# Kernel optimization log

Hardware: AMD Instinct MI355X
Metric: run time of the kernel (lower is better)

The kernel has to match this reference:

```python
import jax, jax.numpy as jnp
import numpy as np

N, F, E = 65536, 64, 16   # batch, fields, embedding_size
H1, H2 = 8, 4             # hidden_dims
BN_EPS = 1e-5


def setup_inputs() -> dict:
    key = jax.random.key(0)
    ks = jax.random.split(key, 12)
    rn = lambda k, shape, sc=1.0: jax.random.normal(k, shape, dtype=jnp.float32) * sc
    return {
        "Xa": rn(ks[0], (N, F)),
        "Xc": rn(ks[1], (N, F)),
        # per-field Linear(1,1) weights/biases (two first-order embedding lists)
        "w1": rn(ks[2], (F,)), "b1": rn(ks[3], (F,)),
        "w2": rn(ks[4], (F,)), "b2": rn(ks[5], (F,)),
        # per-field Linear(1,E) weights/biases (two second-order embedding lists)
        "W1": rn(ks[6], (F, E)), "B1": rn(ks[7], (F, E)),
        "W2": rn(ks[8], (F, E)), "B2": rn(ks[9], (F, E)),
        # deep MLP: linear_1 (F*E -> 8) + BN, linear_2 (8 -> 4). No final layer (init bug).
        "lin1_w": rn(ks[10], (H1, F * E), 0.01), "lin1_b": jnp.zeros((H1,), jnp.float32),
        "bn1_gamma": jnp.ones((H1,), jnp.float32), "bn1_beta": jnp.zeros((H1,), jnp.float32),
        "lin2_w": rn(ks[11], (H2, H1), 0.01), "lin2_b": jnp.full((H2,), 0.21, jnp.float32),
    }


def reference(Xa, Xc, w1, b1, w2, b2, W1, B1, W2, B2,
              lin1_w, lin1_b, bn1_gamma, bn1_beta, lin2_w, lin2_b):
    n = Xa.shape[0]
    # ---- FM first order (faithful to the torch broadcast: arr_2[i] is (N,N)
    # with entry [r,c] = Xa[r,i]*(w2[i]*Xc[c,i]+b2[i]); only mean over the
    # concat dim is consumed, so compute the column-mean analytically). ----
    first1 = (w1 * Xa + b1) * Xc                         # (N,F)
    xc_mean = jnp.mean(Xc, axis=0)                       # (F,)
    first2_cmean = Xa * (w2 * xc_mean + b2)              # (N,F) = mean over c of arr_2
    fm_first_mean = jnp.mean(first1 + first2_cmean, axis=1, keepdims=True)  # (N,1)

    # ---- FM second order: per-field (N,E) embeddings, fully batched. ----
    Xa3 = Xa[:, :, None]                                 # (N,F,1)
    Xc3 = Xc[:, :, None]
    emb = (Xa3 * W1 + B1) * Xc3 + Xa3 * (W2 * Xc3 + B2)  # (N,F,E)
    s = emb.sum(axis=1)                                  # (N,E)
    fm_second = 0.5 * (s * s - (emb * emb).sum(axis=1))  # (N,E)
    fm_second_mean = jnp.mean(fm_second, axis=1, keepdims=True)  # (N,1)

    # ---- deep part: cat of per-field (N,E) -> (N, F*E), field-major. ----
    deep = emb.reshape(n, F * E)
    h = deep @ lin1_w.T + lin1_b                         # (N,8)
    mu = h.mean(axis=0)
    var = h.var(axis=0)                                  # biased, as BN training mode
    h = (h - mu) / jnp.sqrt(var + BN_EPS) * bn1_gamma + bn1_beta
    h = jnp.tanh(h)                                      # dropout = identity (eval)
    h = h @ lin2_w.T + lin2_b                            # (N,4) — no final projection (init bug)
    deep_mean = h.mean(axis=1, keepdims=True)            # (N,1)

    return fm_first_mean + fm_second_mean + deep_mean    # (N,1)
```

## Files before the change

kernel.cpp:

```cpp
#include <hip/hip_runtime.h>
#include <math.h>

#define NROWS 65536
#define BN_EPS 1e-5f
#define NBLK   512

#define OFF_PARTIAL 0
#define OFF_H       65536
#define OFF_REC     589824
#define OFF_BLKT    595200
#define OFF_T       636160

__global__ __launch_bounds__(64) void precompute_kernel(
    const float* __restrict__ W1, const float* __restrict__ B1,
    const float* __restrict__ W2, const float* __restrict__ B2,
    const float* __restrict__ lin1_w, const float* __restrict__ w1,
    const float* __restrict__ b1, const float* __restrict__ b2,
    float* __restrict__ rec)
{
    int f = blockIdx.x, t = threadIdx.x;
    __shared__ float u[16], x[16], y[16];
    if (t < 16) {
        float uu = W1[f * 16 + t] + W2[f * 16 + t];
        float xx = B1[f * 16 + t];
        float yy = B2[f * 16 + t];
        u[t] = uu; x[t] = xx; y[t] = yy;
        rec[f * 84 + t]      = uu;
        rec[f * 84 + 16 + t] = xx;
        rec[f * 84 + 32 + t] = yy;
    }
    __syncthreads();
    if (t < 24) {
        int j = t & 7, which = t >> 3;
        const float* src = (which == 0) ? u : (which == 1) ? x : y;
        const float* lw = lin1_w + j * 1024 + f * 16;
        float acc = 0.f;
#pragma unroll
        for (int e = 0; e < 16; e++) acc = fmaf(src[e], lw[e], acc);
        rec[f * 84 + 48 + which * 8 + j] = acc;
    } else if (t < 30) {
        int q = t - 24;
        const float* s1 = (q == 0 || q == 3 || q == 4) ? u : (q == 1 || q == 5) ? x : y;
        const float* s2 = (q == 0) ? u : (q == 1 || q == 3) ? x : y;
        float acc = 0.f;
#pragma unroll
        for (int e = 0; e < 16; e++) acc = fmaf(s1[e], s2[e], acc);
        rec[f * 84 + 72 + q] = (q < 3 ? 1.f : 2.f) * acc;
    } else if (t == 30) {
        rec[f * 84 + 78] = w1[f];
        rec[f * 84 + 79] = b1[f];
        rec[f * 84 + 80] = b2[f];
        rec[f * 84 + 81] = 0.f;
        rec[f * 84 + 82] = 0.f;
        rec[f * 84 + 83] = 0.f;
    }
}

__global__ __launch_bounds__(256)
__attribute__((amdgpu_waves_per_eu(2, 4)))
void main_kernel(
    const float* __restrict__ Xa, const float* __restrict__ Xc,
    const float* __restrict__ rec, const float* __restrict__ lin1_b,
    float* __restrict__ ws_partial, float* __restrict__ ws_h,
    float* __restrict__ ws_blkT)
{
    __shared__ float cmb[4][64][29];
    __shared__ float scol[256];

    int tid  = threadIdx.x;
    int lane = tid & 63;
    int wv   = tid >> 6;
    int wu   = __builtin_amdgcn_readfirstlane(wv);
    int blk  = blockIdx.x;
    int f0   = wu * 16;
    int rowbase = blk * 128;

    {
        int col = tid & 63, grp = tid >> 6;
        float acc = 0.f;
        for (int r = grp; r < 128; r += 4)
            acc += Xc[(size_t)(rowbase + r) * 64 + col];
        scol[tid] = acc;
    }
    __syncthreads();
    if (tid < 64) {
        float t = scol[tid] + scol[64 + tid] + scol[128 + tid] + scol[192 + tid];
        ws_blkT[(size_t)tid * NBLK + blk] = t;
    }

    size_t rb0 = ((size_t)rowbase + lane) * 64 + f0;
    const float4* pa0 = (const float4*)(Xa + rb0);
    const float4* pc0 = (const float4*)(Xc + rb0);
    const float4* pa1 = (const float4*)(Xa + rb0 + 64 * 64);
    const float4* pc1 = (const float4*)(Xc + rb0 + 64 * 64);

    float s0[16], s1[16], h0[8], h1[8];
#pragma unroll
    for (int e = 0; e < 16; e++) { s0[e] = 0.f; s1[e] = 0.f; }
#pragma unroll
    for (int j = 0; j < 8; j++) { h0[j] = 0.f; h1[j] = 0.f; }
    float p1a = 0.f, p1b = 0.f, p2a0 = 0.f, p2a1 = 0.f, q0 = 0.f, q1 = 0.f;

    const float* recw = rec + (size_t)f0 * 84;
#pragma unroll
    for (int k = 0; k < 4; k++) {
        float4 A0 = pa0[k], C0 = pc0[k];
        float4 A1 = pa1[k], C1 = pc1[k];
        float av0[4] = {A0.x, A0.y, A0.z, A0.w};
        float cv0[4] = {C0.x, C0.y, C0.z, C0.w};
        float av1[4] = {A1.x, A1.y, A1.z, A1.w};
        float cv1[4] = {C1.x, C1.y, C1.z, C1.w};
#pragma unroll
        for (int uu = 0; uu < 4; uu++) {
            const float* r = recw + (k * 4 + uu) * 84;
            {
                float a = av0[uu], c = cv0[uu], pp = a * c;
                p1a  = fmaf(fmaf(r[78], a, r[79]), c, p1a);
                p2a0 = fmaf(a, r[80], p2a0);
                q0 = fmaf(pp * pp, r[72], q0);
                q0 = fmaf(c * c,   r[73], q0);
                q0 = fmaf(a * a,   r[74], q0);
                q0 = fmaf(pp * c,  r[75], q0);
                q0 = fmaf(pp * a,  r[76], q0);
                q0 = fmaf(pp,      r[77], q0);
#pragma unroll
                for (int e = 0; e < 16; e++)
                    s0[e] = fmaf(pp, r[e], fmaf(c, r[16+e], fmaf(a, r[32+e], s0[e])));
#pragma unroll
                for (int j = 0; j < 8; j++)
                    h0[j] = fmaf(pp, r[48+j], fmaf(c, r[56+j], fmaf(a, r[64+j], h0[j])));
            }
            {
                float a = av1[uu], c = cv1[uu], pp = a * c;
                p1b  = fmaf(fmaf(r[78], a, r[79]), c, p1b);
                p2a1 = fmaf(a, r[80], p2a1);
                q1 = fmaf(pp * pp, r[72], q1);
                q1 = fmaf(c * c,   r[73], q1);
                q1 = fmaf(a * a,   r[74], q1);
                q1 = fmaf(pp * c,  r[75], q1);
                q1 = fmaf(pp * a,  r[76], q1);
                q1 = fmaf(pp,      r[77], q1);
#pragma unroll
                for (int e = 0; e < 16; e++)
                    s1[e] = fmaf(pp, r[e], fmaf(c, r[16+e], fmaf(a, r[32+e], s1[e])));
#pragma unroll
                for (int j = 0; j < 8; j++)
                    h1[j] = fmaf(pp, r[48+j], fmaf(c, r[56+j], fmaf(a, r[64+j], h1[j])));
            }
        }
    }

    float bn[16];
#pragma unroll
    for (int i = 0; i < 16; i++) bn[i] = 0.f;

#pragma unroll
    for (int g = 0; g < 2; g++) {
        __syncthreads();
#pragma unroll
        for (int e = 0; e < 16; e++) cmb[wv][lane][e] = g ? s1[e] : s0[e];
#pragma unroll
        for (int j = 0; j < 8; j++) cmb[wv][lane][16 + j] = g ? h1[j] : h0[j];
        cmb[wv][lane][24] = g ? p1b : p1a;
        cmb[wv][lane][25] = g ? p2a1 : p2a0;
        cmb[wv][lane][26] = g ? q1 : q0;
        __syncthreads();

        if (tid < 64) {
            float S[16], H[8], P1 = 0.f, P2 = 0.f, Q = 0.f;
#pragma unroll
            for (int e = 0; e < 16; e++) S[e] = 0.f;
#pragma unroll
            for (int j = 0; j < 8; j++) H[j] = 0.f;
#pragma unroll
            for (int w = 0; w < 4; w++) {
#pragma unroll
                for (int e = 0; e < 16; e++) S[e] += cmb[w][tid][e];
#pragma unroll
                for (int j = 0; j < 8; j++) H[j] += cmb[w][tid][16 + j];
                P1 += cmb[w][tid][24];
                P2 += cmb[w][tid][25];
                Q  += cmb[w][tid][26];
            }
#pragma unroll
            for (int j = 0; j < 8; j++) H[j] += lin1_b[j];

            float ss = 0.f;
#pragma unroll
            for (int e = 0; e < 16; e++) ss = fmaf(S[e], S[e], ss);
            int rr = rowbase + g * 64 + tid;
            ws_partial[rr] = (P1 + P2) * (1.f / 64.f) + (ss - Q) * (0.5f / 16.f);
            *(float4*)(ws_h + (size_t)rr * 8)     = make_float4(H[0], H[1], H[2], H[3]);
            *(float4*)(ws_h + (size_t)rr * 8 + 4) = make_float4(H[4], H[5], H[6], H[7]);
#pragma unroll
            for (int j = 0; j < 8; j++) {
                bn[j]     += H[j];
                bn[8 + j] += H[j] * H[j];
            }
        }
    }

    if (tid < 64) {
#pragma unroll
        for (int off = 1; off < 64; off <<= 1) {
#pragma unroll
            for (int i = 0; i < 16; i++) bn[i] += __shfl_xor(bn[i], off);
        }
        if (tid == 0) {
#pragma unroll
            for (int i = 0; i < 16; i++)
                ws_blkT[(size_t)(64 + i) * NBLK + blk] = bn[i];
        }
    }
}

__global__ __launch_bounds__(256) void reduce_kernel(
    const float* __restrict__ ws_blkT, float* __restrict__ T)
{
    int gtid = blockIdx.x * 256 + threadIdx.x;
    int v = gtid >> 6;
    int lane = gtid & 63;
    const float* p = ws_blkT + (size_t)v * NBLK + lane;
    float acc = 0.f;
#pragma unroll
    for (int k = 0; k < 8; k++) acc += p[k * 64];
#pragma unroll
    for (int off = 32; off; off >>= 1) acc += __shfl_xor(acc, off);
    if (lane == 0) T[v] = acc;
}

__global__ __launch_bounds__(256) void final_kernel(
    const float* __restrict__ Xa, const float* __restrict__ w2,
    const float* __restrict__ gamma, const float* __restrict__ beta,
    const float* __restrict__ lin2_w, const float* __restrict__ lin2_b,
    const float* __restrict__ T, const float* __restrict__ ws_partial,
    const float* __restrict__ ws_h, float* __restrict__ out)
{
    __shared__ float sg[64], sScale[8], sShift[8], sColw[8];
    __shared__ float sBsum;
    int tid = threadIdx.x;
    if (tid < 64) {
        sg[tid] = w2[tid] * (T[tid] * (1.f / 65536.f));
    } else if (tid < 72) {
        int j = tid - 64;
        float mu  = T[64 + j] * (1.f / 65536.f);
        float var = T[72 + j] * (1.f / 65536.f) - mu * mu;
        float sc = gamma[j] / sqrtf(var + BN_EPS);
        sScale[j] = sc;
        sShift[j] = beta[j] - mu * sc;
    } else if (tid < 80) {
        int j = tid - 72;
        sColw[j] = lin2_w[j] + lin2_w[8 + j] + lin2_w[16 + j] + lin2_w[24 + j];
    } else if (tid == 80) {
        sBsum = lin2_b[0] + lin2_b[1] + lin2_b[2] + lin2_b[3];
    }
    __syncthreads();

    int row  = (blockIdx.x * 256 + tid) >> 1;
    int half = tid & 1;
    int fo   = half * 32;

    const float4* xa4 = (const float4*)(Xa + (size_t)row * 64 + fo);
    float p2b = 0.f;
#pragma unroll
    for (int k = 0; k < 8; k++) {
        float4 vv = xa4[k];
        int b = fo + k * 4;
        p2b += vv.x * sg[b] + vv.y * sg[b + 1] + vv.z * sg[b + 2] + vv.w * sg[b + 3];
    }

    float4 hq = *(const float4*)(ws_h + (size_t)row * 8 + half * 4);
    float hv[4] = {hq.x, hq.y, hq.z, hq.w};
    float dmp = 0.f;
#pragma unroll
    for (int jj = 0; jj < 4; jj++) {
        int j = half * 4 + jj;
        float hn = tanhf(hv[jj] * sScale[j] + sShift[j]);
        dmp = fmaf(hn, sColw[j], dmp);
    }

    float val = p2b * (1.f / 64.f) + dmp * 0.25f;
    val += __shfl_xor(val, 1);
    if (!half)
        out[row] = val + ws_partial[row] + sBsum * 0.25f;
}

extern "C" void kernel_launch(void* const* d_in, const int* in_sizes, int n_in,
                              void* d_out, int out_size, void* d_ws, size_t ws_size,
                              hipStream_t stream) {
    const float* Xa        = (const float*)d_in[0];
    const float* Xc        = (const float*)d_in[1];
    const float* w1        = (const float*)d_in[2];
    const float* b1        = (const float*)d_in[3];
    const float* w2        = (const float*)d_in[4];
    const float* b2        = (const float*)d_in[5];
    const float* W1        = (const float*)d_in[6];
    const float* B1        = (const float*)d_in[7];
    const float* W2        = (const float*)d_in[8];
    const float* B2        = (const float*)d_in[9];
    const float* lin1_w    = (const float*)d_in[10];
    const float* lin1_b    = (const float*)d_in[11];
    const float* bn1_gamma = (const float*)d_in[12];
    const float* bn1_beta  = (const float*)d_in[13];
    const float* lin2_w    = (const float*)d_in[14];
    const float* lin2_b    = (const float*)d_in[15];

    float* ws  = (float*)d_ws;
    float* out = (float*)d_out;

    float* ws_partial = ws + OFF_PARTIAL;
    float* ws_h       = ws + OFF_H;
    float* ws_rec     = ws + OFF_REC;
    float* ws_blkT    = ws + OFF_BLKT;
    float* ws_T       = ws + OFF_T;

    precompute_kernel<<<64, 64, 0, stream>>>(W1, B1, W2, B2, lin1_w,
                                             w1, b1, b2, ws_rec);
    main_kernel<<<NBLK, 256, 0, stream>>>(Xa, Xc, ws_rec, lin1_b,
                                          ws_partial, ws_h, ws_blkT);
    reduce_kernel<<<20, 256, 0, stream>>>(ws_blkT, ws_T);
    final_kernel<<<512, 256, 0, stream>>>(Xa, w2, bn1_gamma, bn1_beta,
                                          lin2_w, lin2_b, ws_T,
                                          ws_partial, ws_h, out);
}
```

Baseline: 130.6 us.

## Precompute Xc column means upfront and fold first-order term into main pass

A new column-sum kernel and an extended prep kernel now compute the Xc column means before the main pass. The w2*mean coefficient is stored in the per-field record, so the main kernel folds the second first-order term into its accumulators. This stops the final kernel from re-reading all of Xa. The per-field record table is also staged into shared memory, and the field loop is no longer unrolled, to cut global and scalar loads and register pressure. In exchange the main kernel now waits on an extra kernel that reads Xc one more time, and the loop is less unrolled.

```diff
diff --git a/kernel.cpp b/kernel.cpp
--- a/kernel.cpp
+++ b/kernel.cpp
@@ -8,17 +8,49 @@
 #define OFF_PARTIAL 0
 #define OFF_H       65536
 #define OFF_REC     589824
-#define OFF_BLKT    595200
-#define OFF_T       636160
-
-__global__ __launch_bounds__(64) void precompute_kernel(
+#define OFF_CS      595200
+#define OFF_BLKT    611584
+#define OFF_T       619776
+#define OFF_T2      619840
+
+__global__ __launch_bounds__(256) void colsum_kernel(
+    const float* __restrict__ Xc, float* __restrict__ cs)
+{
+    __shared__ float scol[256];
+    int tid = threadIdx.x, blk = blockIdx.x;
+    int rowbase = blk * 256;
+    int col = tid & 63, grp = tid >> 6;
+    float acc = 0.f;
+    for (int r = grp; r < 256; r += 4)
+        acc += Xc[(size_t)(rowbase + r) * 64 + col];
+    scol[tid] = acc;
+    __syncthreads();
+    if (tid < 64)
+        cs[(size_t)tid * 256 + blk] =
+            scol[tid] + scol[64 + tid] + scol[128 + tid] + scol[192 + tid];
+}
+
+__global__ __launch_bounds__(64) void prep_kernel(
     const float* __restrict__ W1, const float* __restrict__ B1,
     const float* __restrict__ W2, const float* __restrict__ B2,
     const float* __restrict__ lin1_w, const float* __restrict__ w1,
     const float* __restrict__ b1, const float* __restrict__ b2,
-    float* __restrict__ rec)
+    const float* __restrict__ w2, const float* __restrict__ cs,
+    float* __restrict__ rec, float* __restrict__ T)
 {
     int f = blockIdx.x, t = threadIdx.x;
+    if (f == 64) {
+        const float4* p = (const float4*)(cs + (size_t)t * 256);
+        float4 s4 = make_float4(0.f, 0.f, 0.f, 0.f);
+        for (int k = 0; k < 64; k++) {
+            float4 v = p[k];
+            s4.x += v.x; s4.y += v.y; s4.z += v.z; s4.w += v.w;
+        }
+        float sum = (s4.x + s4.y) + (s4.z + s4.w);
+        T[t] = sum;
+        rec[t * 84 + 81] = w2[t] * (sum * (1.f / 65536.f));
+        return;
+    }
     __shared__ float u[16], x[16], y[16];
     if (t < 16) {
         float uu = W1[f * 16 + t] + W2[f * 16 + t];
@@ -50,7 +82,6 @@
         rec[f * 84 + 78] = w1[f];
         rec[f * 84 + 79] = b1[f];
         rec[f * 84 + 80] = b2[f];
-        rec[f * 84 + 81] = 0.f;
         rec[f * 84 + 82] = 0.f;
         rec[f * 84 + 83] = 0.f;
     }
@@ -64,8 +95,7 @@
     float* __restrict__ ws_partial, float* __restrict__ ws_h,
     float* __restrict__ ws_blkT)
 {
-    __shared__ float cmb[4][64][29];
-    __shared__ float scol[256];
+    __shared__ __align__(16) float smem[7424];
 
     int tid  = threadIdx.x;
     int lane = tid & 63;
@@ -76,17 +106,11 @@
     int rowbase = blk * 128;
 
     {
-        int col = tid & 63, grp = tid >> 6;
-        float acc = 0.f;
-        for (int r = grp; r < 128; r += 4)
-            acc += Xc[(size_t)(rowbase + r) * 64 + col];
-        scol[tid] = acc;
+        const float4* src = (const float4*)rec;
+        float4* dst = (float4*)smem;
+        for (int i = tid; i < 1344; i += 256) dst[i] = src[i];
     }
     __syncthreads();
-    if (tid < 64) {
-        float t = scol[tid] + scol[64 + tid] + scol[128 + tid] + scol[192 + tid];
-        ws_blkT[(size_t)tid * NBLK + blk] = t;
-    }
 
     size_t rb0 = ((size_t)rowbase + lane) * 64 + f0;
     const float4* pa0 = (const float4*)(Xa + rb0);
@@ -99,10 +123,11 @@
     for (int e = 0; e < 16; e++) { s0[e] = 0.f; s1[e] = 0.f; }
 #pragma unroll
     for (int j = 0; j < 8; j++) { h0[j] = 0.f; h1[j] = 0.f; }
-    float p1a = 0.f, p1b = 0.f, p2a0 = 0.f, p2a1 = 0.f, q0 = 0.f, q1 = 0.f;
-
-    const float* recw = rec + (size_t)f0 * 84;
-#pragma unroll
+    float p1a = 0.f, p1b = 0.f, p2a0 = 0.f, p2a1 = 0.f;
+    float pb0 = 0.f, pb1 = 0.f, q0 = 0.f, q1 = 0.f;
+
+    const float* recw = smem + f0 * 84;
+#pragma unroll 1
     for (int k = 0; k < 4; k++) {
         float4 A0 = pa0[k], C0 = pc0[k];
         float4 A1 = pa1[k], C1 = pc1[k];
@@ -117,6 +142,7 @@
                 float a = av0[uu], c = cv0[uu], pp = a * c;
                 p1a  = fmaf(fmaf(r[78], a, r[79]), c, p1a);
                 p2a0 = fmaf(a, r[80], p2a0);
+                pb0  = fmaf(a, r[81], pb0);
                 q0 = fmaf(pp * pp, r[72], q0);
                 q0 = fmaf(c * c,   r[73], q0);
                 q0 = fmaf(a * a,   r[74], q0);
@@ -134,6 +160,7 @@
                 float a = av1[uu], c = cv1[uu], pp = a * c;
                 p1b  = fmaf(fmaf(r[78], a, r[79]), c, p1b);
                 p2a1 = fmaf(a, r[80], p2a1);
+                pb1  = fmaf(a, r[81], pb1);
                 q1 = fmaf(pp * pp, r[72], q1);
                 q1 = fmaf(c * c,   r[73], q1);
                 q1 = fmaf(a * a,   r[74], q1);
@@ -157,30 +184,36 @@
 #pragma unroll
     for (int g = 0; g < 2; g++) {
         __syncthreads();
-#pragma unroll
-        for (int e = 0; e < 16; e++) cmb[wv][lane][e] = g ? s1[e] : s0[e];
-#pragma unroll
-        for (int j = 0; j < 8; j++) cmb[wv][lane][16 + j] = g ? h1[j] : h0[j];
-        cmb[wv][lane][24] = g ? p1b : p1a;
-        cmb[wv][lane][25] = g ? p2a1 : p2a0;
-        cmb[wv][lane][26] = g ? q1 : q0;
+        {
+            float* cmb = smem + (wv * 64 + lane) * 29;
+#pragma unroll
+            for (int e = 0; e < 16; e++) cmb[e] = g ? s1[e] : s0[e];
+#pragma unroll
+            for (int j = 0; j < 8; j++) cmb[16 + j] = g ? h1[j] : h0[j];
+            cmb[24] = g ? p1b : p1a;
+            cmb[25] = g ? p2a1 : p2a0;
+            cmb[26] = g ? q1 : q0;
+            cmb[27] = g ? pb1 : pb0;
+        }
         __syncthreads();
 
         if (tid < 64) {
-            float S[16], H[8], P1 = 0.f, P2 = 0.f, Q = 0.f;
+            float S[16], H[8], P1 = 0.f, P2 = 0.f, Q = 0.f, PB = 0.f;
 #pragma unroll
             for (int e = 0; e < 16; e++) S[e] = 0.f;
 #pragma unroll
             for (int j = 0; j < 8; j++) H[j] = 0.f;
 #pragma unroll
             for (int w = 0; w < 4; w++) {
-#pragma unroll
-                for (int e = 0; e < 16; e++) S[e] += cmb[w][tid][e];
-#pragma unroll
-                for (int j = 0; j < 8; j++) H[j] += cmb[w][tid][16 + j];
-                P1 += cmb[w][tid][24];
-                P2 += cmb[w][tid][25];
-                Q  += cmb[w][tid][26];
+                const float* c2 = smem + (w * 64 + tid) * 29;
+#pragma unroll
+                for (int e = 0; e < 16; e++) S[e] += c2[e];
+#pragma unroll
+                for (int j = 0; j < 8; j++) H[j] += c2[16 + j];
+                P1 += c2[24];
+                P2 += c2[25];
+                Q  += c2[26];
+                PB += c2[27];
             }
 #pragma unroll
             for (int j = 0; j < 8; j++) H[j] += lin1_b[j];
@@ -189,7 +222,7 @@
 #pragma unroll
             for (int e = 0; e < 16; e++) ss = fmaf(S[e], S[e], ss);
             int rr = rowbase + g * 64 + tid;
-            ws_partial[rr] = (P1 + P2) * (1.f / 64.f) + (ss - Q) * (0.5f / 16.f);
+            ws_partial[rr] = (P1 + P2 + PB) * (1.f / 64.f) + (ss - Q) * (0.5f / 16.f);
             *(float4*)(ws_h + (size_t)rr * 8)     = make_float4(H[0], H[1], H[2], H[3]);
             *(float4*)(ws_h + (size_t)rr * 8 + 4) = make_float4(H[4], H[5], H[6], H[7]);
 #pragma unroll
@@ -209,13 +242,13 @@
         if (tid == 0) {
 #pragma unroll
             for (int i = 0; i < 16; i++)
-                ws_blkT[(size_t)(64 + i) * NBLK + blk] = bn[i];
-        }
-    }
-}
-
-__global__ __launch_bounds__(256) void reduce_kernel(
-    const float* __restrict__ ws_blkT, float* __restrict__ T)
+                ws_blkT[(size_t)i * NBLK + blk] = bn[i];
+        }
+    }
+}
+
+__global__ __launch_bounds__(256) void bnreduce_kernel(
+    const float* __restrict__ ws_blkT, float* __restrict__ T2)
 {
     int gtid = blockIdx.x * 256 + threadIdx.x;
     int v = gtid >> 6;
@@ -226,63 +259,43 @@
     for (int k = 0; k < 8; k++) acc += p[k * 64];
 #pragma unroll
     for (int off = 32; off; off >>= 1) acc += __shfl_xor(acc, off);
-    if (lane == 0) T[v] = acc;
+    if (lane == 0) T2[v] = acc;
 }
 
 __global__ __launch_bounds__(256) void final_kernel(
-    const float* __restrict__ Xa, const float* __restrict__ w2,
     const float* __restrict__ gamma, const float* __restrict__ beta,
     const float* __restrict__ lin2_w, const float* __restrict__ lin2_b,
-    const float* __restrict__ T, const float* __restrict__ ws_partial,
+    const float* __restrict__ T2, const float* __restrict__ ws_partial,
     const float* __restrict__ ws_h, float* __restrict__ out)
 {
-    __shared__ float sg[64], sScale[8], sShift[8], sColw[8];
+    __shared__ float sScale[8], sShift[8], sColw[8];
     __shared__ float sBsum;
     int tid = threadIdx.x;
-    if (tid < 64) {
-        sg[tid] = w2[tid] * (T[tid] * (1.f / 65536.f));
-    } else if (tid < 72) {
-        int j = tid - 64;
-        float mu  = T[64 + j] * (1.f / 65536.f);
-        float var = T[72 + j] * (1.f / 65536.f) - mu * mu;
-        float sc = gamma[j] / sqrtf(var + BN_EPS);
-        sScale[j] = sc;
-        sShift[j] = beta[j] - mu * sc;
-    } else if (tid < 80) {
-        int j = tid - 72;
+    if (tid < 8) {
+        float mu  = T2[tid] * (1.f / 65536.f);
+        float var = T2[8 + tid] * (1.f / 65536.f) - mu * mu;
+        float sc = gamma[tid] / sqrtf(var + BN_EPS);
+        sScale[tid] = sc;
+        sShift[tid] = beta[tid] - mu * sc;
+    } else if (tid < 16) {
+        int j = tid - 8;
         sColw[j] = lin2_w[j] + lin2_w[8 + j] + lin2_w[16 + j] + lin2_w[24 + j];
-    } else if (tid == 80) {
+    } else if (tid == 16) {
         sBsum = lin2_b[0] + lin2_b[1] + lin2_b[2] + lin2_b[3];
     }
     __syncthreads();
 
-    int row  = (blockIdx.x * 256 + tid) >> 1;
-    int half = tid & 1;
-    int fo   = half * 32;
-
-    const float4* xa4 = (const float4*)(Xa + (size_t)row * 64 + fo);
-    float p2b = 0.f;
-#pragma unroll
-    for (int k = 0; k < 8; k++) {
-        float4 vv = xa4[k];
-        int b = fo + k * 4;
-        p2b += vv.x * sg[b] + vv.y * sg[b + 1] + vv.z * sg[b + 2] + vv.w * sg[b + 3];
-    }
-
-    float4 hq = *(const float4*)(ws_h + (size_t)row * 8 + half * 4);
-    float hv[4] = {hq.x, hq.y, hq.z, hq.w};
-    float dmp = 0.f;
-#pragma unroll
-    for (int jj = 0; jj < 4; jj++) {
-        int j = half * 4 + jj;
-        float hn = tanhf(hv[jj] * sScale[j] + sShift[j]);
-        dmp = fmaf(hn, sColw[j], dmp);
-    }
-
-    float val = p2b * (1.f / 64.f) + dmp * 0.25f;
-    val += __shfl_xor(val, 1);
-    if (!half)
-        out[row] = val + ws_partial[row] + sBsum * 0.25f;
+    int row = blockIdx.x * 256 + tid;
+    float4 h0 = *(const float4*)(ws_h + (size_t)row * 8);
+    float4 h1 = *(const float4*)(ws_h + (size_t)row * 8 + 4);
+    float hv[8] = {h0.x, h0.y, h0.z, h0.w, h1.x, h1.y, h1.z, h1.w};
+    float dm = 0.f;
+#pragma unroll
+    for (int j = 0; j < 8; j++) {
+        float hn = tanhf(hv[j] * sScale[j] + sShift[j]);
+        dm = fmaf(hn, sColw[j], dm);
+    }
+    out[row] = ws_partial[row] + (dm + sBsum) * 0.25f;
 }
 
 extern "C" void kernel_launch(void* const* d_in, const int* in_sizes, int n_in,
@@ -311,15 +324,18 @@
     float* ws_partial = ws + OFF_PARTIAL;
     float* ws_h       = ws + OFF_H;
     float* ws_rec     = ws + OFF_REC;
+    float* ws_cs      = ws + OFF_CS;
     float* ws_blkT    = ws + OFF_BLKT;
     float* ws_T       = ws + OFF_T;
-
-    precompute_kernel<<<64, 64, 0, stream>>>(W1, B1, W2, B2, lin1_w,
-                                             w1, b1, b2, ws_rec);
+    float* ws_T2      = ws + OFF_T2;
+
+    colsum_kernel<<<256, 256, 0, stream>>>(Xc, ws_cs);
+    prep_kernel<<<65, 64, 0, stream>>>(W1, B1, W2, B2, lin1_w,
+                                       w1, b1, b2, w2, ws_cs, ws_rec, ws_T);
     main_kernel<<<NBLK, 256, 0, stream>>>(Xa, Xc, ws_rec, lin1_b,
                                           ws_partial, ws_h, ws_blkT);
-    reduce_kernel<<<20, 256, 0, stream>>>(ws_blkT, ws_T);
-    final_kernel<<<512, 256, 0, stream>>>(Xa, w2, bn1_gamma, bn1_beta,
-                                          lin2_w, lin2_b, ws_T,
+    bnreduce_kernel<<<4, 256, 0, stream>>>(ws_blkT, ws_T2);
+    final_kernel<<<256, 256, 0, stream>>>(bn1_gamma, bn1_beta,
+                                          lin2_w, lin2_b, ws_T2,
                                           ws_partial, ws_h, out);
 }
```

Result: slower. 143.0 us (+9.5%).
